# Optimization experiments

Measured on AMD Instinct MI355X. Metric: run time of the kernel, lower is better.

## Reference

```python
import jax, jax.numpy as jnp
import numpy as np

B, C, H, K = 1024, 1000, 768, 128

def setup_inputs() -> dict:
    key = jax.random.key(0)
    k1, k2, k3, k4 = jax.random.split(key, 4)
    x = jax.random.normal(k1, (B, H), dtype=jnp.float32)
    y = jax.random.randint(k2, (B,), 0, C)
    class_weights = jax.random.normal(k3, (C, H, K), dtype=jnp.float32) * 0.1
    class_bias = jnp.zeros((C, H), dtype=jnp.float32)
    # torch.nn.Linear default init (uniform in +/- 1/sqrt(H))
    bound = 1.0 / np.sqrt(H)
    W_lin = jax.random.uniform(k4, (H, H), dtype=jnp.float32, minval=-bound, maxval=bound)
    b_lin = jnp.zeros((H,), dtype=jnp.float32)
    return {"x": x, "y": y, "class_weights": class_weights,
            "class_bias": class_bias, "W_lin": W_lin, "b_lin": b_lin}

def reference(x, y, class_weights, class_bias, W_lin, b_lin):
    # one-hot matmul gather == true indexed gather (same math)
    weights = class_weights[y]                # [B, H, K]
    neg_x = jax.nn.relu(-x)                   # [B, H]
    x1 = jnp.tanh(neg_x @ W_lin.T + b_lin)    # [B, H]
    # x1[B,1,H] @ weights[B,H,K] -> sum over singleton dim == [B, K]
    logits = jnp.einsum('bh,bhk->bk', x1, weights)
    return logits
```

## Files before the change

kernel.cpp:

```cpp
#include <hip/hip_runtime.h>
#include <hip/hip_bf16.h>
#include <cstddef>

#define B_SZ 1024
#define C_SZ 1000
#define H_SZ 768
#define K_SZ 128

typedef __attribute__((ext_vector_type(8))) short bf16x8;
typedef __attribute__((ext_vector_type(4))) float f32x4;

#define WS_NEGX_OFF 0
#define WS_W_OFF    1572864
#define WS_X1_OFF   4194304

__global__ __launch_bounds__(256) void convert_pack(
    const float* __restrict__ x, const float* __restrict__ W,
    ushort* __restrict__ negx, ushort* __restrict__ Wb)
{
    const int NX = B_SZ * H_SZ / 4;
    const int NW = H_SZ * H_SZ / 4;
    int i = blockIdx.x * 256 + threadIdx.x;
    if (i < NX) {
        float4 v = ((const float4*)x)[i];
        union { ushort u[4]; ushort4 v4; } o;
        o.u[0] = __bfloat16_as_ushort(__float2bfloat16(fmaxf(-v.x, 0.f)));
        o.u[1] = __bfloat16_as_ushort(__float2bfloat16(fmaxf(-v.y, 0.f)));
        o.u[2] = __bfloat16_as_ushort(__float2bfloat16(fmaxf(-v.z, 0.f)));
        o.u[3] = __bfloat16_as_ushort(__float2bfloat16(fmaxf(-v.w, 0.f)));
        ((ushort4*)negx)[i] = o.v4;
    } else {
        int j = i - NX;
        if (j < NW) {
            float4 v = ((const float4*)W)[j];
            union { ushort u[4]; ushort4 v4; } o;
            o.u[0] = __bfloat16_as_ushort(__float2bfloat16(v.x));
            o.u[1] = __bfloat16_as_ushort(__float2bfloat16(v.y));
            o.u[2] = __bfloat16_as_ushort(__float2bfloat16(v.z));
            o.u[3] = __bfloat16_as_ushort(__float2bfloat16(v.w));
            ((ushort4*)Wb)[j] = o.v4;
        }
    }
}

__global__ __launch_bounds__(256) void mfma_gemm_tanh(
    const ushort* __restrict__ A, const ushort* __restrict__ Bw,
    const float* __restrict__ bias, float* __restrict__ x1)
{
    const int LDA = 40;
    __shared__ ushort sA[64 * LDA];
    __shared__ ushort sB[64 * LDA];

    const int t    = threadIdx.x;
    const int wave = t >> 6;
    const int lane = t & 63;
    const int wm   = wave >> 1;
    const int wn   = wave & 1;
    const int m0   = blockIdx.y * 64;
    const int n0   = blockIdx.x * 64;

    const int lr = t >> 2;
    const int lc = (t & 3) * 8;

    f32x4 acc[2][2] = {};

    const int fr = lane & 15;
    const int fk = (lane >> 4) * 8;

    for (int k0 = 0; k0 < H_SZ; k0 += 32) {
        *(bf16x8*)(&sA[lr * LDA + lc]) =
            *(const bf16x8*)(&A[(size_t)(m0 + lr) * H_SZ + k0 + lc]);
        *(bf16x8*)(&sB[lr * LDA + lc]) =
            *(const bf16x8*)(&Bw[(size_t)(n0 + lr) * H_SZ + k0 + lc]);
        __syncthreads();

        #pragma unroll
        for (int fi = 0; fi < 2; ++fi) {
            bf16x8 af = *(const bf16x8*)(&sA[(wm * 32 + fi * 16 + fr) * LDA + fk]);
            #pragma unroll
            for (int fj = 0; fj < 2; ++fj) {
                bf16x8 bf = *(const bf16x8*)(&sB[(wn * 32 + fj * 16 + fr) * LDA + fk]);
                acc[fi][fj] = __builtin_amdgcn_mfma_f32_16x16x32_bf16(
                    af, bf, acc[fi][fj], 0, 0, 0);
            }
        }
        __syncthreads();
    }

    const int col   = lane & 15;
    const int rbase = (lane >> 4) * 4;
    #pragma unroll
    for (int fi = 0; fi < 2; ++fi) {
        #pragma unroll
        for (int fj = 0; fj < 2; ++fj) {
            const int n  = n0 + wn * 32 + fj * 16 + col;
            const float bv = bias[n];
            #pragma unroll
            for (int r = 0; r < 4; ++r) {
                const int m = m0 + wm * 32 + fi * 16 + rbase + r;
                x1[(size_t)m * H_SZ + n] = tanhf(acc[fi][fj][r] + bv);
            }
        }
    }
}

__global__ __launch_bounds__(256) void gather_dot(
    const float* __restrict__ x1, const int* __restrict__ y,
    const float* __restrict__ cw, float* __restrict__ out)
{
    const int b   = blockIdx.x;
    const int t   = threadIdx.x;
    const int k4  = t & 31;
    const int hg  = t >> 5;

    __shared__ float sx[H_SZ];
    __shared__ float4 red[256];

    const int cls = y[b];
    const float4* __restrict__ wrow =
        (const float4*)(cw + (size_t)cls * H_SZ * K_SZ);

    for (int i = t; i < H_SZ; i += 256)
        sx[i] = x1[(size_t)b * H_SZ + i];
    __syncthreads();

    float4 acc = {0.f, 0.f, 0.f, 0.f};
    #pragma unroll 4
    for (int h = hg; h < H_SZ; h += 8) {
        const float  xv = sx[h];
        const float4 w  = wrow[h * 32 + k4];
        acc.x += xv * w.x;
        acc.y += xv * w.y;
        acc.z += xv * w.z;
        acc.w += xv * w.w;
    }

    red[t] = acc;
    __syncthreads();
    if (t < 128) {
        float4 o = red[t + 128];
        red[t].x += o.x; red[t].y += o.y; red[t].z += o.z; red[t].w += o.w;
    }
    __syncthreads();
    if (t < 64) {
        float4 o = red[t + 64];
        red[t].x += o.x; red[t].y += o.y; red[t].z += o.z; red[t].w += o.w;
    }
    __syncthreads();
    if (t < 32) {
        float4 r = red[t];
        float4 o = red[t + 32];
        r.x += o.x; r.y += o.y; r.z += o.z; r.w += o.w;
        ((float4*)out)[(size_t)b * 32 + t] = r;
    }
}

extern "C" void kernel_launch(void* const* d_in, const int* in_sizes, int n_in,
                              void* d_out, int out_size, void* d_ws, size_t ws_size,
                              hipStream_t stream) {
    const float* x    = (const float*)d_in[0];
    const int*   y    = (const int*)  d_in[1];
    const float* cw   = (const float*)d_in[2];
    const float* Wlin = (const float*)d_in[4];
    const float* blin = (const float*)d_in[5];
    float* out = (float*)d_out;

    char* ws = (char*)d_ws;
    ushort* negx = (ushort*)(ws + WS_NEGX_OFF);
    ushort* Wb   = (ushort*)(ws + WS_W_OFF);
    float*  x1   = (float*) (ws + WS_X1_OFF);

    const int total4 = (B_SZ * H_SZ + H_SZ * H_SZ) / 4;
    convert_pack<<<(total4 + 255) / 256, 256, 0, stream>>>(x, Wlin, negx, Wb);

    dim3 g1(H_SZ / 64, B_SZ / 64);
    mfma_gemm_tanh<<<g1, 256, 0, stream>>>(negx, Wb, blin, x1);

    gather_dot<<<B_SZ, 256, 0, stream>>>(x1, y, cw, out);
}
```

Before: 511.4 us.

## Group batch rows by class so each class weight slab is read once

Adds a small counting pass and a bucketing pass that group batch indices by label. The gather-dot kernel is then launched once per class instead of once per sample, so each class's H×K weight slab is streamed from memory once and reused for up to four samples at a time. This targets the duplicated weight traffic when several samples share a label. In exchange it adds two tiny kernel launches and an atomic histogram. Buckets are capped at 16 samples per class, so any extra samples of an over-full class would silently get no output.

```diff
diff --git a/kernel.cpp b/kernel.cpp
--- a/kernel.cpp
+++ b/kernel.cpp
@@ -6,6 +6,8 @@
 #define C_SZ 1000
 #define H_SZ 768
 #define K_SZ 128
+#define MAXS 16
+#define CHUNK 4
 
 typedef __attribute__((ext_vector_type(8))) short bf16x8;
 typedef __attribute__((ext_vector_type(4))) float f32x4;
@@ -13,6 +15,8 @@
 #define WS_NEGX_OFF 0
 #define WS_W_OFF    1572864
 #define WS_X1_OFF   4194304
+#define WS_CNT_OFF  8388608
+#define WS_BKT_OFF  8392704
 
 __global__ __launch_bounds__(256) void convert_pack(
     const float* __restrict__ x, const float* __restrict__ W,
@@ -104,54 +108,83 @@
     }
 }
 
-__global__ __launch_bounds__(256) void gather_dot(
-    const float* __restrict__ x1, const int* __restrict__ y,
-    const float* __restrict__ cw, float* __restrict__ out)
-{
-    const int b   = blockIdx.x;
-    const int t   = threadIdx.x;
-    const int k4  = t & 31;
-    const int hg  = t >> 5;
-
-    __shared__ float sx[H_SZ];
-    __shared__ float4 red[256];
-
-    const int cls = y[b];
+__global__ __launch_bounds__(256) void init_counts(int* __restrict__ counts)
+{
+    for (int i = threadIdx.x; i < C_SZ; i += 256) counts[i] = 0;
+}
+
+__global__ __launch_bounds__(256) void build_buckets(
+    const int* __restrict__ y, int* __restrict__ counts,
+    int* __restrict__ buckets)
+{
+    const int b = blockIdx.x * 256 + threadIdx.x;
+    if (b < B_SZ) {
+        const int cls  = y[b];
+        const int slot = atomicAdd(&counts[cls], 1);
+        if (slot < MAXS) buckets[cls * MAXS + slot] = b;
+    }
+}
+
+__global__ __launch_bounds__(256) void gather_dot_dedup(
+    const float* __restrict__ x1, const int* __restrict__ counts,
+    const int* __restrict__ buckets, const float* __restrict__ cw,
+    float* __restrict__ out)
+{
+    const int c = blockIdx.x;
+    int n = counts[c];
+    if (n == 0) return;
+    if (n > MAXS) n = MAXS;
+
+    const int t  = threadIdx.x;
+    const int k4 = t & 31;
+    const int hg = t >> 5;
+
+    __shared__ float  sx[CHUNK][H_SZ];
+    __shared__ float4 red[8][32];
+    __shared__ int    sb[CHUNK];
+
     const float4* __restrict__ wrow =
-        (const float4*)(cw + (size_t)cls * H_SZ * K_SZ);
-
-    for (int i = t; i < H_SZ; i += 256)
-        sx[i] = x1[(size_t)b * H_SZ + i];
-    __syncthreads();
-
-    float4 acc = {0.f, 0.f, 0.f, 0.f};
-    #pragma unroll 4
-    for (int h = hg; h < H_SZ; h += 8) {
-        const float  xv = sx[h];
-        const float4 w  = wrow[h * 32 + k4];
-        acc.x += xv * w.x;
-        acc.y += xv * w.y;
-        acc.z += xv * w.z;
-        acc.w += xv * w.w;
-    }
-
-    red[t] = acc;
-    __syncthreads();
-    if (t < 128) {
-        float4 o = red[t + 128];
-        red[t].x += o.x; red[t].y += o.y; red[t].z += o.z; red[t].w += o.w;
-    }
-    __syncthreads();
-    if (t < 64) {
-        float4 o = red[t + 64];
-        red[t].x += o.x; red[t].y += o.y; red[t].z += o.z; red[t].w += o.w;
-    }
-    __syncthreads();
-    if (t < 32) {
-        float4 r = red[t];
-        float4 o = red[t + 32];
-        r.x += o.x; r.y += o.y; r.z += o.z; r.w += o.w;
-        ((float4*)out)[(size_t)b * 32 + t] = r;
+        (const float4*)(cw + (size_t)c * H_SZ * K_SZ);
+
+    for (int s0 = 0; s0 < n; s0 += CHUNK) {
+        const int m = min(CHUNK, n - s0);
+        if (t < m) sb[t] = buckets[c * MAXS + s0 + t];
+        __syncthreads();
+        for (int s = 0; s < m; ++s) {
+            const int b = sb[s];
+            for (int i = t; i < H_SZ; i += 256)
+                sx[s][i] = x1[(size_t)b * H_SZ + i];
+        }
+        __syncthreads();
+
+        float4 acc[CHUNK] = {};
+        #pragma unroll 8
+        for (int h = hg; h < H_SZ; h += 8) {
+            const float4 w = wrow[h * 32 + k4];
+            #pragma unroll
+            for (int s = 0; s < CHUNK; ++s) {
+                const float xv = sx[s][h];
+                acc[s].x += xv * w.x;
+                acc[s].y += xv * w.y;
+                acc[s].z += xv * w.z;
+                acc[s].w += xv * w.w;
+            }
+        }
+
+        for (int s = 0; s < m; ++s) {
+            red[hg][k4] = acc[s];
+            __syncthreads();
+            if (hg == 0) {
+                float4 r = red[0][k4];
+                #pragma unroll
+                for (int g = 1; g < 8; ++g) {
+                    float4 o = red[g][k4];
+                    r.x += o.x; r.y += o.y; r.z += o.z; r.w += o.w;
+                }
+                ((float4*)out)[(size_t)sb[s] * 32 + k4] = r;
+            }
+            __syncthreads();
+        }
     }
 }
 
@@ -166,15 +199,20 @@
     float* out = (float*)d_out;
 
     char* ws = (char*)d_ws;
-    ushort* negx = (ushort*)(ws + WS_NEGX_OFF);
-    ushort* Wb   = (ushort*)(ws + WS_W_OFF);
-    float*  x1   = (float*) (ws + WS_X1_OFF);
+    ushort* negx  = (ushort*)(ws + WS_NEGX_OFF);
+    ushort* Wb    = (ushort*)(ws + WS_W_OFF);
+    float*  x1    = (float*) (ws + WS_X1_OFF);
+    int*    cnts  = (int*)   (ws + WS_CNT_OFF);
+    int*    bkts  = (int*)   (ws + WS_BKT_OFF);
 
     const int total4 = (B_SZ * H_SZ + H_SZ * H_SZ) / 4;
     convert_pack<<<(total4 + 255) / 256, 256, 0, stream>>>(x, Wlin, negx, Wb);
 
+    init_counts<<<1, 256, 0, stream>>>(cnts);
+    build_buckets<<<B_SZ / 256, 256, 0, stream>>>(y, cnts, bkts);
+
     dim3 g1(H_SZ / 64, B_SZ / 64);
     mfma_gemm_tanh<<<g1, 256, 0, stream>>>(negx, Wb, blin, x1);
 
-    gather_dot<<<B_SZ, 256, 0, stream>>>(x1, y, cw, out);
-}
+    gather_dot_dedup<<<C_SZ, 256, 0, stream>>>(x1, cnts, bkts, cw, out);
+}
```

Result: slower. 552.3 us (+8.0%).

## Split gather-dot over two H halves with a separate combine kernel

Applied to the files above, without the earlier changes.

Launches the gather/dot stage with twice as many blocks, each covering half of the hidden dimension. Partial results go to workspace and a new kernel adds them. The loop unroll rises from 4 to 8, and the reduction becomes a single-wave sum over 8 groups. The aim is more memory-level parallelism on the large class-weight reads, at the cost of an extra launch and partial-sum traffic.

```diff
diff --git a/kernel.cpp b/kernel.cpp
--- a/kernel.cpp
+++ b/kernel.cpp
@@ -13,6 +13,7 @@
 #define WS_NEGX_OFF 0
 #define WS_W_OFF    1572864
 #define WS_X1_OFF   4194304
+#define WS_PART_OFF 8388608
 
 __global__ __launch_bounds__(256) void convert_pack(
     const float* __restrict__ x, const float* __restrict__ W,
@@ -104,29 +105,32 @@
     }
 }
 
-__global__ __launch_bounds__(256) void gather_dot(
+__global__ __launch_bounds__(256) void gather_dot_split(
     const float* __restrict__ x1, const int* __restrict__ y,
-    const float* __restrict__ cw, float* __restrict__ out)
+    const float* __restrict__ cw, float* __restrict__ part)
 {
-    const int b   = blockIdx.x;
-    const int t   = threadIdx.x;
-    const int k4  = t & 31;
-    const int hg  = t >> 5;
+    const int HH   = H_SZ / 2;
+    const int b    = blockIdx.x;
+    const int half = blockIdx.y;
+    const int t    = threadIdx.x;
+    const int k4   = t & 31;
+    const int hg   = t >> 5;
+    const int h0   = half * HH;
 
-    __shared__ float sx[H_SZ];
-    __shared__ float4 red[256];
+    __shared__ float  sx[HH];
+    __shared__ float4 red[8][32];
 
     const int cls = y[b];
     const float4* __restrict__ wrow =
-        (const float4*)(cw + (size_t)cls * H_SZ * K_SZ);
+        (const float4*)(cw + (size_t)cls * H_SZ * K_SZ) + (size_t)h0 * 32;
 
-    for (int i = t; i < H_SZ; i += 256)
-        sx[i] = x1[(size_t)b * H_SZ + i];
+    for (int i = t; i < HH; i += 256)
+        sx[i] = x1[(size_t)b * H_SZ + h0 + i];
     __syncthreads();
 
     float4 acc = {0.f, 0.f, 0.f, 0.f};
-    #pragma unroll 4
-    for (int h = hg; h < H_SZ; h += 8) {
+    #pragma unroll 8
+    for (int h = hg; h < HH; h += 8) {
         const float  xv = sx[h];
         const float4 w  = wrow[h * 32 + k4];
         acc.x += xv * w.x;
@@ -135,23 +139,29 @@
         acc.w += xv * w.w;
     }
 
-    red[t] = acc;
+    red[hg][k4] = acc;
     __syncthreads();
-    if (t < 128) {
-        float4 o = red[t + 128];
-        red[t].x += o.x; red[t].y += o.y; red[t].z += o.z; red[t].w += o.w;
+    if (hg == 0) {
+        float4 r = red[0][k4];
+        #pragma unroll
+        for (int g = 1; g < 8; ++g) {
+            float4 o = red[g][k4];
+            r.x += o.x; r.y += o.y; r.z += o.z; r.w += o.w;
+        }
+        ((float4*)part)[((size_t)half * B_SZ + b) * 32 + k4] = r;
     }
-    __syncthreads();
-    if (t < 64) {
-        float4 o = red[t + 64];
-        red[t].x += o.x; red[t].y += o.y; red[t].z += o.z; red[t].w += o.w;
-    }
-    __syncthreads();
-    if (t < 32) {
-        float4 r = red[t];
-        float4 o = red[t + 32];
-        r.x += o.x; r.y += o.y; r.z += o.z; r.w += o.w;
-        ((float4*)out)[(size_t)b * 32 + t] = r;
+}
+
+__global__ __launch_bounds__(256) void combine_halves(
+    const float* __restrict__ part, float* __restrict__ out)
+{
+    const int N4 = B_SZ * K_SZ / 4;
+    int i = blockIdx.x * 256 + threadIdx.x;
+    if (i < N4) {
+        float4 a = ((const float4*)part)[i];
+        float4 b = ((const float4*)part)[N4 + i];
+        float4 r = {a.x + b.x, a.y + b.y, a.z + b.z, a.w + b.w};
+        ((float4*)out)[i] = r;
     }
 }
 
@@ -169,6 +179,7 @@
     ushort* negx = (ushort*)(ws + WS_NEGX_OFF);
     ushort* Wb   = (ushort*)(ws + WS_W_OFF);
     float*  x1   = (float*) (ws + WS_X1_OFF);
+    float*  part = (float*) (ws + WS_PART_OFF);
 
     const int total4 = (B_SZ * H_SZ + H_SZ * H_SZ) / 4;
     convert_pack<<<(total4 + 255) / 256, 256, 0, stream>>>(x, Wlin, negx, Wb);
@@ -176,5 +187,8 @@
     dim3 g1(H_SZ / 64, B_SZ / 64);
     mfma_gemm_tanh<<<g1, 256, 0, stream>>>(negx, Wb, blin, x1);
 
-    gather_dot<<<B_SZ, 256, 0, stream>>>(x1, y, cw, out);
+    dim3 g2(B_SZ, 2);
+    gather_dot_split<<<g2, 256, 0, stream>>>(x1, y, cw, part);
+
+    combine_halves<<<(B_SZ * K_SZ / 4 + 255) / 256, 256, 0, stream>>>(part, out);
 }
```

After: 516.5 us. Within noise of the previous version (+1.0%).
